# Performance work log

Measured on AMD Instinct MI355X. Metric: run time of the kernel, lower is better.

The kernel has to match this reference:

```python
import jax, jax.numpy as jnp
import numpy as np

THETA = 10000.0

def _rope_cos_sin(seq_len, head_dim, dtype=jnp.float32):
    # matches precompute_freqs_cis: freqs over even indices of head_dim
    inv = 1.0 / (THETA ** (jnp.arange(0, head_dim, 2, dtype=jnp.float32) / head_dim))  # [hd/2]
    ang = jnp.arange(seq_len, dtype=jnp.float32)[:, None] * inv[None, :]               # [S, hd/2]
    return jnp.cos(ang).astype(dtype), jnp.sin(ang).astype(dtype)

def _apply_rope(x, cos, sin):
    # x: [b, h, s, d]; pairs are interleaved (d r) with r=2 -> complex (even=real, odd=imag)
    xe = x[..., 0::2]
    xo = x[..., 1::2]
    re = xe * cos - xo * sin
    im = xe * sin + xo * cos
    # interleave back: [..., d/2, 2] -> [..., d]
    return jnp.stack([re, im], axis=-1).reshape(x.shape)

def setup_inputs() -> dict:
    key = jax.random.key(0)
    ks = jax.random.split(key, 8)
    B, S, D = 2, 2048, 1024
    s = 0.02
    return {
        "query": jax.random.normal(ks[0], (B, S, D), jnp.float32),
        "key": jax.random.normal(ks[1], (B, S, D), jnp.float32),
        "value": jax.random.normal(ks[2], (B, S, D), jnp.float32),
        "q_w": jax.random.normal(ks[3], (D, D), jnp.float32) * s,
        "q_b": jnp.zeros((D,), jnp.float32),
        "k_w": jax.random.normal(ks[4], (D, D), jnp.float32) * s,
        "k_b": jnp.zeros((D,), jnp.float32),
        "v_w": jax.random.normal(ks[5], (D, D), jnp.float32) * s,
        "v_b": jnp.zeros((D,), jnp.float32),
        "o_w": jax.random.normal(ks[6], (D, D), jnp.float32) * s,
        "o_b": jnp.zeros((D,), jnp.float32),
    }

def reference(query, key, value, q_w, q_b, k_w, k_b, v_w, v_b, o_w, o_b):
    H = 16
    B, S, D = query.shape
    hd = D // H
    scaling = hd ** -0.5

    def split_heads(x):  # [b, s, (h d)] -> [b, h, s, d]
        return x.reshape(B, -1, H, hd).transpose(0, 2, 1, 3)

    q = split_heads(query @ q_w.T + q_b)
    k = split_heads(key @ k_w.T + k_b)
    v = split_heads(value @ v_w.T + v_b)

    cos, sin = _rope_cos_sin(S, hd)
    q = _apply_rope(q, cos, sin)
    k = _apply_rope(k, cos, sin)

    scores = jnp.einsum('bhqd,bhkd->bhqk', q, k) * scaling  # [B,H,S,S]
    attn = jax.nn.softmax(scores, axis=-1)
    out = jnp.einsum('bhqk,bhkd->bhqd', attn, v)            # [B,H,S,hd]
    out = out.transpose(0, 2, 1, 3).reshape(B, S, D)
    return out @ o_w.T + o_b
```

## Files before the change

### kernel.cpp

```cpp
#include <hip/hip_runtime.h>
#include <math.h>

#define B_  2
#define S_  2048
#define D_  1024
#define H_  16
#define HD_ 64
#define M_  (B_*S_)

typedef __attribute__((ext_vector_type(8))) short bf16x8;
typedef __attribute__((ext_vector_type(4))) float f32x4;
typedef unsigned short ushort_t;

#define MFMA32 __builtin_amdgcn_mfma_f32_16x16x32_bf16

__device__ inline unsigned short f2bf(float x) {
    unsigned u = __float_as_uint(x);
    unsigned r = (u + 0x7fff + ((u >> 16) & 1)) >> 16;
    return (unsigned short)r;
}
__device__ inline void gload16(const ushort_t* g, ushort_t* l) {
    __builtin_amdgcn_global_load_lds(
        (const __attribute__((address_space(1))) unsigned*)g,
        (__attribute__((address_space(3))) unsigned*)l, 16, 0, 0);
}

__global__ __launch_bounds__(256) void prep(
    const float* __restrict__ qa, const float* __restrict__ ka,
    const float* __restrict__ va,
    const float* __restrict__ qw, const float* __restrict__ kw,
    const float* __restrict__ vw, const float* __restrict__ ow,
    ushort_t* __restrict__ qab, ushort_t* __restrict__ kab,
    ushort_t* __restrict__ vab,
    ushort_t* __restrict__ qwb, ushort_t* __restrict__ kwb,
    ushort_t* __restrict__ vwb, ushort_t* __restrict__ owb,
    float* __restrict__ cost, float* __restrict__ sint)
{
    const int z = blockIdx.y;
    const int i = blockIdx.x * 256 + threadIdx.x;
    if (z == 7) {
        if (blockIdx.x >= (S_ * 32) / 256) return;
        int s = i >> 5, w = i & 31;
        double inv = pow(10000.0, -((double)(2 * w) / (double)HD_));
        double ang = (double)s * inv;
        cost[i] = (float)cos(ang);
        sint[i] = (float)sin(ang);
        return;
    }
    const float* in;
    ushort_t* dst;
    int n4;
    switch (z) {
        case 0: in = qa; dst = qab; n4 = (M_ * D_) / 4; break;
        case 1: in = ka; dst = kab; n4 = (M_ * D_) / 4; break;
        case 2: in = va; dst = vab; n4 = (M_ * D_) / 4; break;
        case 3: in = qw; dst = qwb; n4 = (D_ * D_) / 4; break;
        case 4: in = kw; dst = kwb; n4 = (D_ * D_) / 4; break;
        case 5: in = vw; dst = vwb; n4 = (D_ * D_) / 4; break;
        default: in = ow; dst = owb; n4 = (D_ * D_) / 4; break;
    }
    if (i >= n4) return;
    float4 v = ((const float4*)in)[i];
    unsigned short h0 = f2bf(v.x), h1 = f2bf(v.y), h2 = f2bf(v.z), h3 = f2bf(v.w);
    ((uint2*)dst)[i] = make_uint2((unsigned)h0 | ((unsigned)h1 << 16),
                                  (unsigned)h2 | ((unsigned)h3 << 16));
}

__global__ __launch_bounds__(256, 3) void fused_qkv(
    const ushort_t* __restrict__ A0, const ushort_t* __restrict__ A1,
    const ushort_t* __restrict__ A2,
    const ushort_t* __restrict__ W0, const ushort_t* __restrict__ W1,
    const ushort_t* __restrict__ W2,
    const float* __restrict__ b0, const float* __restrict__ b1,
    const float* __restrict__ b2,
    ushort_t* __restrict__ O0, ushort_t* __restrict__ O1,
    ushort_t* __restrict__ O2,
    const float* __restrict__ cost, const float* __restrict__ sint)
{
    __shared__ ushort_t Ab[12288];
    __shared__ ushort_t Wb[12288];

    const int tid  = threadIdx.x;
    const int wq   = tid >> 6;
    const int lane = tid & 63;
    const int l16  = lane & 15;
    const int quad = lane >> 4;

    const unsigned flat = blockIdx.x + (blockIdx.y << 3) + (blockIdx.z << 8);
    const unsigned xcd  = flat & 7;
    const unsigned slot = flat >> 3;
    const int z   = (int)(slot >> 5);
    const unsigned rr = slot & 31;
    const int bm  = (int)(xcd * 4 + (rr >> 3)) * 128;
    const int bn  = (int)(rr & 7) * 128;

    const ushort_t* A = z == 0 ? A0 : z == 1 ? A1 : A2;
    const ushort_t* W = z == 0 ? W0 : z == 1 ? W1 : W2;
    const float* bias = z == 0 ? b0 : z == 1 ? b1 : b2;

    const int m16 = tid & 15;
    const int akq = (tid >> 4) & 3;
    const int tw  = tid >> 6;

    const ushort_t* gA0 = A + (size_t)(bm + tw * 16 + m16) * D_ + akq * 8;
    const ushort_t* gA1 = gA0 + (size_t)64 * D_;
    const ushort_t* gW0 = W + (size_t)(bn + tw * 16 + m16) * D_ + akq * 8;
    const ushort_t* gW1 = gW0 + (size_t)64 * D_;

    const int wm = wq >> 1, wn = wq & 1;

    f32x4 acc[4][4];
#pragma unroll
    for (int mt = 0; mt < 4; ++mt)
#pragma unroll
        for (int nt = 0; nt < 4; ++nt)
            acc[mt][nt] = (f32x4){0.f, 0.f, 0.f, 0.f};

    gload16(gA0,      &Ab[tw * 512]);
    gload16(gA1,      &Ab[(tw + 4) * 512]);
    gload16(gW0,      &Wb[tw * 512]);
    gload16(gW1,      &Wb[(tw + 4) * 512]);
    gload16(gA0 + 32, &Ab[4096 + tw * 512]);
    gload16(gA1 + 32, &Ab[4096 + (tw + 4) * 512]);
    gload16(gW0 + 32, &Wb[4096 + tw * 512]);
    gload16(gW1 + 32, &Wb[4096 + (tw + 4) * 512]);

    int bcur = 0;
    for (int k = 0; k < 32; ++k) {
        if (k < 31) {
            asm volatile("s_waitcnt vmcnt(4)" ::: "memory");
        } else {
            asm volatile("s_waitcnt vmcnt(0)" ::: "memory");
        }
        __builtin_amdgcn_sched_barrier(0);
        __builtin_amdgcn_s_barrier();
        __builtin_amdgcn_sched_barrier(0);

        if (k < 30) {
            int bnx = bcur + 2; if (bnx >= 3) bnx -= 3;
            int ko = (k + 2) * 32;
            gload16(gA0 + ko, &Ab[bnx * 4096 + tw * 512]);
            gload16(gA1 + ko, &Ab[bnx * 4096 + (tw + 4) * 512]);
            gload16(gW0 + ko, &Wb[bnx * 4096 + tw * 512]);
            gload16(gW1 + ko, &Wb[bnx * 4096 + (tw + 4) * 512]);
        }

        const ushort_t* Abc = &Ab[bcur * 4096];
        const ushort_t* Wbc = &Wb[bcur * 4096];

        bf16x8 af[4], wf[4];
#pragma unroll
        for (int mt = 0; mt < 4; ++mt)
            af[mt] = *(const bf16x8*)&Abc[(wm * 4 + mt) * 512 + lane * 8];
#pragma unroll
        for (int nt = 0; nt < 4; ++nt)
            wf[nt] = *(const bf16x8*)&Wbc[(wn * 4 + nt) * 512 + lane * 8];
#pragma unroll
        for (int mt = 0; mt < 4; ++mt)
#pragma unroll
            for (int nt = 0; nt < 4; ++nt)
                acc[mt][nt] = MFMA32(af[mt], wf[nt], acc[mt][nt], 0, 0, 0);

        bcur += 1; if (bcur >= 3) bcur -= 3;
    }

    if (z == 0) {
        const float scale = 0.18033688011112042f;
#pragma unroll
        for (int mt = 0; mt < 4; ++mt) {
            int m = bm + wm * 64 + mt * 16 + quad * 4;
#pragma unroll
            for (int nt = 0; nt < 4; ++nt) {
                int n = bn + wn * 64 + nt * 16 + l16;
                float bb = bias[n];
                int h = n >> 6, d = n & 63, p = d >> 1;
#pragma unroll
                for (int r = 0; r < 4; ++r) {
                    int mm = m + r;
                    int s = mm & (S_ - 1), b = mm >> 11;
                    float x = acc[mt][nt][r] + bb;
                    float cs = cost[s * 32 + p], sn = sint[s * 32 + p];
                    float part = __shfl_xor(x, 1);
                    float y = (d & 1) ? (part * sn + x * cs)
                                      : (x * cs - part * sn);
                    O0[((size_t)(b * H_ + h) * S_ + s) * HD_ + d] = f2bf(y * scale);
                }
            }
        }
    } else if (z == 1) {
#pragma unroll
        for (int mt = 0; mt < 4; ++mt) {
            int m = bm + wm * 64 + mt * 16 + quad * 4;
#pragma unroll
            for (int nt = 0; nt < 4; ++nt) {
                int n = bn + wn * 64 + nt * 16 + l16;
                float bb = bias[n];
                int h = n >> 6, d = n & 63, p = d >> 1;
                int sub = ((d >> 5) & 1);
                int dq  = (d >> 3) & 3;
                int dj  = d & 7;
#pragma unroll
                for (int r = 0; r < 4; ++r) {
                    int mm = m + r;
                    int s = mm & (S_ - 1), b = mm >> 11;
                    float x = acc[mt][nt][r] + bb;
                    float cs = cost[s * 32 + p], sn = sint[s * 32 + p];
                    float part = __shfl_xor(x, 1);
                    float y = (d & 1) ? (part * sn + x * cs)
                                      : (x * cs - part * sn);
                    int kt  = s >> 5;
                    int st  = ((s >> 4) & 1) * 2 + sub;
                    size_t idx = ((size_t)(b * H_ + h) * 64 + kt) * 2048
                               + st * 512 + dq * 128 + (s & 15) * 8 + dj;
                    O1[idx] = f2bf(y);
                }
            }
        }
    } else {
#pragma unroll
        for (int mt = 0; mt < 4; ++mt) {
            int m = bm + wm * 64 + mt * 16 + quad * 4;
            int b = m >> 11, s0 = m & (S_ - 1);
            int vt = s0 >> 5;
            int kk = s0 & 31;
            int qd = (kk & 15) >> 2;
            int w0 = ((kk >> 4) & 1) * 4;
#pragma unroll
            for (int nt = 0; nt < 4; ++nt) {
                int n = bn + wn * 64 + nt * 16 + l16;
                float bb = bias[n];
                int h = n >> 6, d = n & 63;
                int mtv = d >> 4, dd = d & 15;
                unsigned short hh[4];
#pragma unroll
                for (int r = 0; r < 4; ++r)
                    hh[r] = f2bf(acc[mt][nt][r] + bb);
                size_t idx = ((size_t)(b * H_ + h) * 64 + vt) * 2048
                           + mtv * 512 + qd * 128 + dd * 8 + w0;
                *(uint2*)(O2 + idx) = make_uint2(
                    (unsigned)hh[0] | ((unsigned)hh[1] << 16),
                    (unsigned)hh[2] | ((unsigned)hh[3] << 16));
            }
        }
    }
}

__global__ __launch_bounds__(256, 4) void proj_o(
    const ushort_t* __restrict__ A, const ushort_t* __restrict__ W,
    const float* __restrict__ bias, float* __restrict__ outf)
{
    __shared__ ushort_t Ab[6144];
    __shared__ ushort_t Wb[6144];

    const int tid  = threadIdx.x;
    const int wq   = tid >> 6;
    const int lane = tid & 63;
    const int l16  = lane & 15;
    const int quad = lane >> 4;

    const unsigned flat = blockIdx.x + (blockIdx.y << 4);
    const unsigned xcd  = flat & 7;
    const unsigned slot = flat >> 3;
    const int bm = (int)(xcd * 8 + (slot >> 4)) * 64;
    const int bn = (int)(slot & 15) * 64;

    const int m16 = tid & 15;
    const int akq = (tid >> 4) & 3;
    const int tw  = tid >> 6;

    const ushort_t* gA = A + (size_t)(bm + tw * 16 + m16) * D_ + akq * 8;
    const ushort_t* gW = W + (size_t)(bn + tw * 16 + m16) * D_ + akq * 8;

    const int wm = wq >> 1, wn = wq & 1;

    f32x4 acc[2][2];
#pragma unroll
    for (int mt = 0; mt < 2; ++mt)
#pragma unroll
        for (int nt = 0; nt < 2; ++nt)
            acc[mt][nt] = (f32x4){0.f, 0.f, 0.f, 0.f};

    gload16(gA,      &Ab[tw * 512]);
    gload16(gW,      &Wb[tw * 512]);
    gload16(gA + 32, &Ab[2048 + tw * 512]);
    gload16(gW + 32, &Wb[2048 + tw * 512]);

    int bcur = 0;
    for (int k = 0; k < 32; ++k) {
        if (k < 31) {
            asm volatile("s_waitcnt vmcnt(2)" ::: "memory");
        } else {
            asm volatile("s_waitcnt vmcnt(0)" ::: "memory");
        }
        __builtin_amdgcn_sched_barrier(0);
        __builtin_amdgcn_s_barrier();
        __builtin_amdgcn_sched_barrier(0);

        if (k < 30) {
            int bnx = bcur + 2; if (bnx >= 3) bnx -= 3;
            int ko = (k + 2) * 32;
            gload16(gA + ko, &Ab[bnx * 2048 + tw * 512]);
            gload16(gW + ko, &Wb[bnx * 2048 + tw * 512]);
        }

        const ushort_t* Abc = &Ab[bcur * 2048];
        const ushort_t* Wbc = &Wb[bcur * 2048];

        bf16x8 af[2], wf[2];
#pragma unroll
        for (int mt = 0; mt < 2; ++mt)
            af[mt] = *(const bf16x8*)&Abc[(wm * 2 + mt) * 512 + lane * 8];
#pragma unroll
        for (int nt = 0; nt < 2; ++nt)
            wf[nt] = *(const bf16x8*)&Wbc[(wn * 2 + nt) * 512 + lane * 8];
#pragma unroll
        for (int mt = 0; mt < 2; ++mt)
#pragma unroll
            for (int nt = 0; nt < 2; ++nt)
                acc[mt][nt] = MFMA32(af[mt], wf[nt], acc[mt][nt], 0, 0, 0);

        bcur += 1; if (bcur >= 3) bcur -= 3;
    }

#pragma unroll
    for (int mt = 0; mt < 2; ++mt) {
        int m = bm + wm * 32 + mt * 16 + quad * 4;
#pragma unroll
        for (int nt = 0; nt < 2; ++nt) {
            int n = bn + wn * 32 + nt * 16 + l16;
            float bb = bias[n];
#pragma unroll
            for (int r = 0; r < 4; ++r)
                outf[(size_t)(m + r) * D_ + n] = acc[mt][nt][r] + bb;
        }
    }
}

__device__ __forceinline__ void attn_body(
    bf16x8 (&KR)[4], bf16x8 (&VR)[4], int i,
    const bf16x8 (&qa)[4][2], f32x4 (&oacc)[4][4], f32x4 (&osum)[4],
    const bf16x8& ones8, const ushort_t* kp, const ushort_t* vp)
{
    f32x4 s[4][2];
#pragma unroll
    for (int nh = 0; nh < 4; ++nh)
#pragma unroll
        for (int g = 0; g < 2; ++g)
            s[nh][g] = (f32x4){0.f, 0.f, 0.f, 0.f};
    __builtin_amdgcn_s_setprio(1);
#pragma unroll
    for (int c = 0; c < 2; ++c)
#pragma unroll
        for (int nh = 0; nh < 4; ++nh)
#pragma unroll
            for (int g = 0; g < 2; ++g)
                s[nh][g] = MFMA32(KR[g * 2 + c], qa[nh][c], s[nh][g], 0, 0, 0);
    __builtin_amdgcn_s_setprio(0);

    bf16x8 pb8[4];
#pragma unroll
    for (int nh = 0; nh < 4; ++nh) {
        float p00 = __builtin_exp2f(s[nh][0][0]);
        float p01 = __builtin_exp2f(s[nh][0][1]);
        float p02 = __builtin_exp2f(s[nh][0][2]);
        float p03 = __builtin_exp2f(s[nh][0][3]);
        float p10 = __builtin_exp2f(s[nh][1][0]);
        float p11 = __builtin_exp2f(s[nh][1][1]);
        float p12 = __builtin_exp2f(s[nh][1][2]);
        float p13 = __builtin_exp2f(s[nh][1][3]);
        union { bf16x8 v; unsigned u[4]; } t;
        t.u[0] = __builtin_amdgcn_perm(__float_as_uint(p01),
                                       __float_as_uint(p00), 0x07060302);
        t.u[1] = __builtin_amdgcn_perm(__float_as_uint(p03),
                                       __float_as_uint(p02), 0x07060302);
        t.u[2] = __builtin_amdgcn_perm(__float_as_uint(p11),
                                       __float_as_uint(p10), 0x07060302);
        t.u[3] = __builtin_amdgcn_perm(__float_as_uint(p13),
                                       __float_as_uint(p12), 0x07060302);
        pb8[nh] = t.v;
    }

    __builtin_amdgcn_s_setprio(1);
#pragma unroll
    for (int mt = 0; mt < 4; ++mt)
#pragma unroll
        for (int nh = 0; nh < 4; ++nh)
            oacc[nh][mt] = MFMA32(VR[mt], pb8[nh], oacc[nh][mt], 0, 0, 0);
#pragma unroll
    for (int nh = 0; nh < 4; ++nh)
        osum[nh] = MFMA32(ones8, pb8[nh], osum[nh], 0, 0, 0);
    __builtin_amdgcn_s_setprio(0);

    if (i + 2 < 32) {
#pragma unroll
        for (int j = 0; j < 4; ++j) {
            KR[j] = *(const bf16x8*)(kp + (size_t)(i + 2) * 4096 + j * 512);
            VR[j] = *(const bf16x8*)(vp + (size_t)(i + 2) * 4096 + j * 512);
        }
    }
}

__global__ __launch_bounds__(256, 2) void attn_mfma(
    const ushort_t* __restrict__ Q, const ushort_t* __restrict__ Kf,
    const ushort_t* __restrict__ Vf, ushort_t* __restrict__ AO)
{
    __shared__ float MRG[128 * 65];
    __shared__ float PSB[128];

    const int tid  = threadIdx.x;
    const int wq   = tid >> 6;
    const int lane = tid & 63;
    const int l16  = lane & 15;
    const int quad = lane >> 4;
    const int qg   = wq & 1;
    const int ks   = wq >> 1;

    const unsigned flat = blockIdx.x + (blockIdx.y << 4);
    const unsigned xcd  = flat & 7;
    const unsigned slot = flat >> 3;
    const int bh   = (int)(xcd * 4 + (slot >> 4));
    const int q0   = (int)(slot & 15) * 128 + qg * 64;

    bf16x8 qa[4][2];
#pragma unroll
    for (int nh = 0; nh < 4; ++nh)
#pragma unroll
        for (int c = 0; c < 2; ++c) {
            int row = q0 + nh * 16 + l16;
            qa[nh][c] = *(const bf16x8*)(Q + ((size_t)bh * S_ + row) * HD_
                                           + c * 32 + quad * 8);
        }
#pragma unroll
    for (int nh = 0; nh < 4; ++nh)
#pragma unroll
        for (int c = 0; c < 2; ++c)
            asm volatile("" : "+v"(qa[nh][c]));

    f32x4 oacc[4][4];
    f32x4 osum[4];
#pragma unroll
    for (int nh = 0; nh < 4; ++nh) {
        osum[nh] = (f32x4){0.f, 0.f, 0.f, 0.f};
#pragma unroll
        for (int mt = 0; mt < 4; ++mt)
            oacc[nh][mt] = (f32x4){0.f, 0.f, 0.f, 0.f};
    }

    const bf16x8 ones8 = {(short)0x3F80, (short)0x3F80, (short)0x3F80,
                          (short)0x3F80, (short)0x3F80, (short)0x3F80,
                          (short)0x3F80, (short)0x3F80};

    const ushort_t* kp = Kf + (size_t)bh * 131072 + ks * 2048 + lane * 8;
    const ushort_t* vp = Vf + (size_t)bh * 131072 + ks * 2048 + lane * 8;

    bf16x8 kA[4], vA[4], kB[4], vB[4];
#pragma unroll
    for (int j = 0; j < 4; ++j) {
        kA[j] = *(const bf16x8*)(kp + j * 512);
        vA[j] = *(const bf16x8*)(vp + j * 512);
        kB[j] = *(const bf16x8*)(kp + 4096 + j * 512);
        vB[j] = *(const bf16x8*)(vp + 4096 + j * 512);
    }

    for (int i = 0; i < 32; i += 2) {
        attn_body(kA, vA, i,     qa, oacc, osum, ones8, kp, vp);
        attn_body(kB, vB, i + 1, qa, oacc, osum, ones8, kp, vp);
    }

    if (ks == 1) {
#pragma unroll
        for (int nh = 0; nh < 4; ++nh) {
#pragma unroll
            for (int mt = 0; mt < 4; ++mt)
#pragma unroll
                for (int r = 0; r < 4; ++r)
                    MRG[(qg * 64 + nh * 16 + l16) * 65 + mt * 16 + quad * 4 + r]
                        = oacc[nh][mt][r];
            if (quad == 0)
                PSB[qg * 64 + nh * 16 + l16] = osum[nh][0];
        }
    }
    __syncthreads();
    if (ks == 0) {
        const int b = bh >> 4, h = bh & 15;
#pragma unroll
        for (int nh = 0; nh < 4; ++nh) {
            float pst = osum[nh][0] + PSB[qg * 64 + nh * 16 + l16];
            float inv = 1.0f / pst;
            int q = q0 + nh * 16 + l16;
#pragma unroll
            for (int mt = 0; mt < 4; ++mt) {
                unsigned short hh[4];
#pragma unroll
                for (int r = 0; r < 4; ++r) {
                    float x = oacc[nh][mt][r]
                        + MRG[(qg * 64 + nh * 16 + l16) * 65 + mt * 16 + quad * 4 + r];
                    hh[r] = f2bf(x * inv);
                }
                size_t base = ((size_t)b * S_ + q) * D_ + h * HD_
                            + mt * 16 + quad * 4;
                *(uint2*)(AO + base) = make_uint2(
                    (unsigned)hh[0] | ((unsigned)hh[1] << 16),
                    (unsigned)hh[2] | ((unsigned)hh[3] << 16));
            }
        }
    }
}

extern "C" void kernel_launch(void* const* d_in, const int* in_sizes, int n_in,
                              void* d_out, int out_size, void* d_ws, size_t ws_size,
                              hipStream_t stream) {
    const float* query = (const float*)d_in[0];
    const float* key   = (const float*)d_in[1];
    const float* value = (const float*)d_in[2];
    const float* q_w   = (const float*)d_in[3];
    const float* q_b   = (const float*)d_in[4];
    const float* k_w   = (const float*)d_in[5];
    const float* k_b   = (const float*)d_in[6];
    const float* v_w   = (const float*)d_in[7];
    const float* v_b   = (const float*)d_in[8];
    const float* o_w   = (const float*)d_in[9];
    const float* o_b   = (const float*)d_in[10];
    float* out = (float*)d_out;

    const size_t NT = (size_t)M_ * D_;
    const size_t WT = (size_t)D_ * D_;
    ushort_t* p = (ushort_t*)d_ws;
    ushort_t* qa_b = p; p += NT;
    ushort_t* ka_b = p; p += NT;
    ushort_t* va_b = p; p += NT;
    ushort_t* wqb  = p; p += WT;
    ushort_t* wkb  = p; p += WT;
    ushort_t* wvb  = p; p += WT;
    ushort_t* wob  = p; p += WT;
    ushort_t* Qb   = p; p += NT;
    ushort_t* Kfr  = p; p += NT;
    ushort_t* Vfr  = p; p += NT;
    ushort_t* AO   = p; p += NT;
    float* cost = (float*)p;
    float* sint = cost + (size_t)S_ * 32;

    dim3 gp((unsigned)(NT / 4 / 256), 8);
    prep<<<gp, 256, 0, stream>>>(query, key, value, q_w, k_w, v_w, o_w,
                                 qa_b, ka_b, va_b, wqb, wkb, wvb, wob,
                                 cost, sint);

    dim3 gq(D_ / 128, M_ / 128, 3);
    fused_qkv<<<gq, 256, 0, stream>>>(
        qa_b, ka_b, va_b, wqb, wkb, wvb,
        q_b, k_b, v_b, Qb, Kfr, Vfr, cost, sint);

    dim3 agrid(S_ / 128, B_ * H_);
    attn_mfma<<<agrid, 256, 0, stream>>>(Qb, Kfr, Vfr, AO);

    dim3 go(D_ / 64, M_ / 64);
    proj_o<<<go, 256, 0, stream>>>(AO, wob, o_b, out);
}
```

Before: 253.0 us.

## Load QKV GEMM operands directly from global into registers, dropping LDS staging

The fused QKV projection GEMM no longer stages A and W tiles through shared memory with a triple-buffered async global-to-LDS pipeline and barriers. Each wave now loads its own MFMA fragments straight from global memory into registers, double-buffered across two k-slices. This removes LDS traffic and block-wide synchronisation. In exchange, operands shared between waves are loaded redundantly from global/L2 with less coalesced 16-byte per-lane row accesses, and register pressure rises.

After: 294.9 us. 1.17x slower.

```diff
diff --git a/kernel.cpp b/kernel.cpp
--- a/kernel.cpp
+++ b/kernel.cpp
@@ -77,9 +77,6 @@
     ushort_t* __restrict__ O2,
     const float* __restrict__ cost, const float* __restrict__ sint)
 {
-    __shared__ ushort_t Ab[12288];
-    __shared__ ushort_t Wb[12288];
-
     const int tid  = threadIdx.x;
     const int wq   = tid >> 6;
     const int lane = tid & 63;
@@ -98,16 +95,16 @@
     const ushort_t* W = z == 0 ? W0 : z == 1 ? W1 : W2;
     const float* bias = z == 0 ? b0 : z == 1 ? b1 : b2;
 
-    const int m16 = tid & 15;
-    const int akq = (tid >> 4) & 3;
-    const int tw  = tid >> 6;
-
-    const ushort_t* gA0 = A + (size_t)(bm + tw * 16 + m16) * D_ + akq * 8;
-    const ushort_t* gA1 = gA0 + (size_t)64 * D_;
-    const ushort_t* gW0 = W + (size_t)(bn + tw * 16 + m16) * D_ + akq * 8;
-    const ushort_t* gW1 = gW0 + (size_t)64 * D_;
-
     const int wm = wq >> 1, wn = wq & 1;
+
+    const ushort_t* aAddr[4];
+    const ushort_t* wAddr[4];
+#pragma unroll
+    for (int mt = 0; mt < 4; ++mt)
+        aAddr[mt] = A + (size_t)(bm + wm * 64 + mt * 16 + l16) * D_ + quad * 8;
+#pragma unroll
+    for (int nt = 0; nt < 4; ++nt)
+        wAddr[nt] = W + (size_t)(bn + wn * 64 + nt * 16 + l16) * D_ + quad * 8;
 
     f32x4 acc[4][4];
 #pragma unroll
@@ -116,52 +113,40 @@
         for (int nt = 0; nt < 4; ++nt)
             acc[mt][nt] = (f32x4){0.f, 0.f, 0.f, 0.f};
 
-    gload16(gA0,      &Ab[tw * 512]);
-    gload16(gA1,      &Ab[(tw + 4) * 512]);
-    gload16(gW0,      &Wb[tw * 512]);
-    gload16(gW1,      &Wb[(tw + 4) * 512]);
-    gload16(gA0 + 32, &Ab[4096 + tw * 512]);
-    gload16(gA1 + 32, &Ab[4096 + (tw + 4) * 512]);
-    gload16(gW0 + 32, &Wb[4096 + tw * 512]);
-    gload16(gW1 + 32, &Wb[4096 + (tw + 4) * 512]);
-
-    int bcur = 0;
-    for (int k = 0; k < 32; ++k) {
-        if (k < 31) {
-            asm volatile("s_waitcnt vmcnt(4)" ::: "memory");
-        } else {
-            asm volatile("s_waitcnt vmcnt(0)" ::: "memory");
-        }
-        __builtin_amdgcn_sched_barrier(0);
-        __builtin_amdgcn_s_barrier();
-        __builtin_amdgcn_sched_barrier(0);
-
-        if (k < 30) {
-            int bnx = bcur + 2; if (bnx >= 3) bnx -= 3;
-            int ko = (k + 2) * 32;
-            gload16(gA0 + ko, &Ab[bnx * 4096 + tw * 512]);
-            gload16(gA1 + ko, &Ab[bnx * 4096 + (tw + 4) * 512]);
-            gload16(gW0 + ko, &Wb[bnx * 4096 + tw * 512]);
-            gload16(gW1 + ko, &Wb[bnx * 4096 + (tw + 4) * 512]);
-        }
-
-        const ushort_t* Abc = &Ab[bcur * 4096];
-        const ushort_t* Wbc = &Wb[bcur * 4096];
-
-        bf16x8 af[4], wf[4];
+    bf16x8 aA[4], wA[4], aB[4], wB[4];
+#pragma unroll
+    for (int j = 0; j < 4; ++j) {
+        aA[j] = *(const bf16x8*)(aAddr[j]);
+        wA[j] = *(const bf16x8*)(wAddr[j]);
+        aB[j] = *(const bf16x8*)(aAddr[j] + 32);
+        wB[j] = *(const bf16x8*)(wAddr[j] + 32);
+    }
+
+    for (int k0 = 0; k0 < D_; k0 += 64) {
 #pragma unroll
         for (int mt = 0; mt < 4; ++mt)
-            af[mt] = *(const bf16x8*)&Abc[(wm * 4 + mt) * 512 + lane * 8];
-#pragma unroll
-        for (int nt = 0; nt < 4; ++nt)
-            wf[nt] = *(const bf16x8*)&Wbc[(wn * 4 + nt) * 512 + lane * 8];
+#pragma unroll
+            for (int nt = 0; nt < 4; ++nt)
+                acc[mt][nt] = MFMA32(aA[mt], wA[nt], acc[mt][nt], 0, 0, 0);
+        if (k0 + 64 < D_) {
+#pragma unroll
+            for (int j = 0; j < 4; ++j) {
+                aA[j] = *(const bf16x8*)(aAddr[j] + k0 + 64);
+                wA[j] = *(const bf16x8*)(wAddr[j] + k0 + 64);
+            }
+        }
 #pragma unroll
         for (int mt = 0; mt < 4; ++mt)
 #pragma unroll
             for (int nt = 0; nt < 4; ++nt)
-                acc[mt][nt] = MFMA32(af[mt], wf[nt], acc[mt][nt], 0, 0, 0);
-
-        bcur += 1; if (bcur >= 3) bcur -= 3;
+                acc[mt][nt] = MFMA32(aB[mt], wB[nt], acc[mt][nt], 0, 0, 0);
+        if (k0 + 96 < D_) {
+#pragma unroll
+            for (int j = 0; j < 4; ++j) {
+                aB[j] = *(const bf16x8*)(aAddr[j] + k0 + 96);
+                wB[j] = *(const bf16x8*)(wAddr[j] + k0 + 96);
+            }
+        }
     }
 
     if (z == 0) {
```
